# Performance work log

Measured on AMD Instinct MI355X. Metric: run time of the kernel, lower is better.

The kernel has to match this reference:

```python
import jax, jax.numpy as jnp
import numpy as np

N_HEADS = 32
N_KV_HEADS = 8
HEAD_DIM = 64  # dim // n_heads = 2048 // 32

def setup_inputs() -> dict:
    key = jax.random.key(0)
    k1, k2, k3, k4, k5 = jax.random.split(key, 5)
    B, T, D = 2, 2048, 2048
    s = 0.02
    return {
        "x": jax.random.normal(k1, (B, T, D), dtype=jnp.float32),
        "wq": jax.random.normal(k2, (D, D), dtype=jnp.float32) * s,
        "wk": jax.random.normal(k3, (N_KV_HEADS * HEAD_DIM, D), dtype=jnp.float32) * s,
        "wv": jax.random.normal(k4, (N_KV_HEADS * HEAD_DIM, D), dtype=jnp.float32) * s,
        "wo": jax.random.normal(k5, (D, D), dtype=jnp.float32) * s,
    }

def reference(x, wq, wk, wv, wo):
    B, T, D = x.shape
    ratio = N_HEADS // N_KV_HEADS
    scale = HEAD_DIM ** -0.5
    # projections (nn.Linear: x @ W.T)
    q = (x @ wq.T).reshape(B, T, N_HEADS, HEAD_DIM)
    k = (x @ wk.T).reshape(B, T, N_KV_HEADS, HEAD_DIM)
    v = (x @ wv.T).reshape(B, T, N_KV_HEADS, HEAD_DIM)
    # GQA expand: [B,T,kvh,d] -> [B,T,kvh*ratio,d]
    k = jnp.broadcast_to(k[:, :, :, None, :], (B, T, N_KV_HEADS, ratio, HEAD_DIM)).reshape(B, T, N_HEADS, HEAD_DIM)
    v = jnp.broadcast_to(v[:, :, :, None, :], (B, T, N_KV_HEADS, ratio, HEAD_DIM)).reshape(B, T, N_HEADS, HEAD_DIM)
    # [B,H,T,d]
    q = q.transpose(0, 2, 1, 3)
    k = k.transpose(0, 2, 1, 3)
    v = v.transpose(0, 2, 1, 3)
    # naive full score matrix [B,H,T,T]
    score = jnp.einsum('bhqd,bhkd->bhqk', q, k) * scale
    causal = jnp.triu(jnp.full((T, T), -jnp.inf, dtype=score.dtype), k=1)
    score = score + causal
    # upcast to fp32 for softmax (matches score.float())
    attn = jax.nn.softmax(score.astype(jnp.float32), axis=-1)
    out = jnp.einsum('bhqk,bhkd->bhqd', attn, v.astype(jnp.float32)).astype(x.dtype)
    out = out.transpose(0, 2, 1, 3).reshape(B, T, N_HEADS * HEAD_DIM)
    return out @ wo.T
```

## Files before the change

### kernel.cpp

```cpp
#include <hip/hip_runtime.h>
#include <hip/hip_bf16.h>

typedef unsigned short u16;
typedef unsigned int   u32;
typedef __attribute__((ext_vector_type(8))) short s16x8;
typedef __attribute__((ext_vector_type(4))) float f32x4;

__device__ __forceinline__ u16 f2bf(float f) {
    u32 u = __float_as_uint(f);
    u += 0x7fff + ((u >> 16) & 1);
    return (u16)(u >> 16);
}

__device__ __forceinline__ f32x4 mfma16(s16x8 a, s16x8 b, f32x4 c) {
    return __builtin_amdgcn_mfma_f32_16x16x32_bf16(a, b, c, 0, 0, 0);
}

#define GLL16(g, l)                                                            \
    __builtin_amdgcn_global_load_lds(                                          \
        (const __attribute__((address_space(1))) void*)(g),                    \
        (__attribute__((address_space(3))) void*)(l), 16, 0, 0)

__global__ void cvt_f32_bf16(const float* __restrict__ src, u16* __restrict__ dst, int n8) {
    int i = blockIdx.x * blockDim.x + threadIdx.x;
    if (i >= n8) return;
    const float4* s4 = reinterpret_cast<const float4*>(src);
    float4 a = s4[2 * i], b = s4[2 * i + 1];
    s16x8 o;
    o[0] = (short)f2bf(a.x); o[1] = (short)f2bf(a.y);
    o[2] = (short)f2bf(a.z); o[3] = (short)f2bf(a.w);
    o[4] = (short)f2bf(b.x); o[5] = (short)f2bf(b.y);
    o[6] = (short)f2bf(b.z); o[7] = (short)f2bf(b.w);
    reinterpret_cast<s16x8*>(dst)[i] = o;
}

template <int BF16_OUT>
__global__ __launch_bounds__(256, 2)
void gemm_bt(const u16* __restrict__ A, const u16* __restrict__ B,
             void* __restrict__ Cout, int M, int N, int K) {
    __shared__ __align__(16) u16 As[128 * 32];
    __shared__ __align__(16) u16 Bs[128 * 32];
    const int tid = threadIdx.x;
    const int w = tid >> 6, ln = tid & 63;
    const int m0 = blockIdx.y * 128, n0 = blockIdx.x * 128;
    const int wr = w >> 1, wc = w & 1;
    const int g = ln >> 4, c15 = ln & 15;
    f32x4 acc[4][4] = {};
    const int srow0 = w * 32 + (ln >> 2);
    const int spos = ln & 3;
    for (int k0 = 0; k0 < K; k0 += 32) {
        __syncthreads();
#pragma unroll
        for (int j = 0; j < 2; ++j) {
            int row = srow0 + j * 16;
            int ch = spos ^ ((row >> 1) & 3);
            const u16* ga = A + (size_t)(m0 + row) * K + k0 + ch * 8;
            GLL16(ga, (char*)As + (w * 32 + j * 16) * 64);
            const u16* gb = B + (size_t)(n0 + row) * K + k0 + ch * 8;
            GLL16(gb, (char*)Bs + (w * 32 + j * 16) * 64);
        }
        __syncthreads();
        s16x8 af[4], bfr[4];
#pragma unroll
        for (int ms = 0; ms < 4; ++ms) {
            int row = wr * 64 + ms * 16 + c15;
            int cp = g ^ ((row >> 1) & 3);
            af[ms] = *reinterpret_cast<const s16x8*>((const char*)As + row * 64 + cp * 16);
        }
#pragma unroll
        for (int ns = 0; ns < 4; ++ns) {
            int row = wc * 64 + ns * 16 + c15;
            int cp = g ^ ((row >> 1) & 3);
            bfr[ns] = *reinterpret_cast<const s16x8*>((const char*)Bs + row * 64 + cp * 16);
        }
        __builtin_amdgcn_s_setprio(1);
#pragma unroll
        for (int ms = 0; ms < 4; ++ms)
#pragma unroll
            for (int ns = 0; ns < 4; ++ns)
                acc[ms][ns] = mfma16(af[ms], bfr[ns], acc[ms][ns]);
        __builtin_amdgcn_s_setprio(0);
    }
#pragma unroll
    for (int ms = 0; ms < 4; ++ms)
#pragma unroll
        for (int ns = 0; ns < 4; ++ns)
#pragma unroll
            for (int r = 0; r < 4; ++r) {
                int row = m0 + wr * 64 + ms * 16 + g * 4 + r;
                int col = n0 + wc * 64 + ns * 16 + c15;
                float v = acc[ms][ns][r];
                if (BF16_OUT)
                    ((u16*)Cout)[(size_t)row * N + col] = f2bf(v);
                else
                    ((float*)Cout)[(size_t)row * N + col] = v;
            }
}

__global__ __launch_bounds__(512, 2)
void attn_fwd(const u16* __restrict__ qkv, u16* __restrict__ outp) {
    const int T = 2048, RS = 3072;
    const int pair = blockIdx.x, kvh = blockIdx.y, b = blockIdx.z;
    const int tid = threadIdx.x, w = tid >> 6, ln = tid & 63;
    const int g = ln >> 4, c15 = ln & 15;
    const int h = kvh * 4 + (w >> 1);
    const int qs = w & 1;
    __shared__ __align__(16) u16 Ks[64 * 64];
    __shared__ __align__(16) u16 Vt[64 * 72];
    __shared__ __align__(16) u16 Ps[8][32 * 72];
    const size_t base = (size_t)b * T * RS;
    const float SCALE2 = 0.125f * 1.44269504088896f;

    for (int ph = 0; ph < 2; ++ph) {
        const int qb = ph ? (31 - pair) : pair;
        const int qg0 = qb * 64 + qs * 32;

        s16x8 qf[2][2];
#pragma unroll
        for (int ms = 0; ms < 2; ++ms)
#pragma unroll
            for (int ks = 0; ks < 2; ++ks)
                qf[ms][ks] = *reinterpret_cast<const s16x8*>(
                    qkv + base + (size_t)(qg0 + ms * 16 + c15) * RS + h * 64 + ks * 32 + g * 8);

        f32x4 o[2][4] = {};
        float mrow[2][4], lrow[2][4];
#pragma unroll
        for (int ms = 0; ms < 2; ++ms)
#pragma unroll
            for (int r = 0; r < 4; ++r) { mrow[ms][r] = -INFINITY; lrow[ms][r] = 0.f; }

        const int nt = qb + 1;
        for (int t = 0; t < nt; ++t) {
            __syncthreads();
            {
                int row = w * 8 + (ln >> 3);
                int ch = (ln & 7) ^ (row & 7);
                const u16* gk = qkv + base + (size_t)(t * 64 + row) * RS + 2048 + kvh * 64 + ch * 8;
                GLL16(gk, (char*)Ks + w * 1024);
            }
            {
                s16x8 vv = *reinterpret_cast<const s16x8*>(
                    qkv + base + (size_t)(t * 64 + ln) * RS + 2560 + kvh * 64 + w * 8);
#pragma unroll
                for (int i = 0; i < 8; ++i)
                    Vt[(w * 8 + i) * 72 + ln] = (u16)vv[i];
            }
            __syncthreads();

            f32x4 s[2][4] = {};
#pragma unroll
            for (int ks = 0; ks < 2; ++ks) {
                s16x8 kf[4];
#pragma unroll
                for (int ns = 0; ns < 4; ++ns) {
                    int row = ns * 16 + c15;
                    int ch = (ks * 4 + g) ^ (row & 7);
                    kf[ns] = *reinterpret_cast<const s16x8*>((const char*)Ks + row * 128 + ch * 16);
                }
                __builtin_amdgcn_s_setprio(1);
#pragma unroll
                for (int ms = 0; ms < 2; ++ms)
#pragma unroll
                    for (int ns = 0; ns < 4; ++ns)
                        s[ms][ns] = mfma16(qf[ms][ks], kf[ns], s[ms][ns]);
                __builtin_amdgcn_s_setprio(0);
            }

#pragma unroll
            for (int ms = 0; ms < 2; ++ms) {
#pragma unroll
                for (int r = 0; r < 4; ++r) {
                    int qrow = qg0 + ms * 16 + g * 4 + r;
                    float mx = -INFINITY;
#pragma unroll
                    for (int ns = 0; ns < 4; ++ns) {
                        int col = t * 64 + ns * 16 + c15;
                        float v = s[ms][ns][r] * SCALE2;
                        v = (col <= qrow) ? v : -INFINITY;
                        s[ms][ns][r] = v;
                        mx = fmaxf(mx, v);
                    }
                    mx = fmaxf(mx, __shfl_xor(mx, 1));
                    mx = fmaxf(mx, __shfl_xor(mx, 2));
                    mx = fmaxf(mx, __shfl_xor(mx, 4));
                    mx = fmaxf(mx, __shfl_xor(mx, 8));
                    float mold = mrow[ms][r];
                    float mnew = fmaxf(mold, mx);
                    float fac = exp2f(mold - mnew);
                    float rsum = 0.f;
#pragma unroll
                    for (int ns = 0; ns < 4; ++ns) {
                        float p = exp2f(s[ms][ns][r] - mnew);
                        s[ms][ns][r] = p;
                        rsum += p;
                    }
                    rsum += __shfl_xor(rsum, 1);
                    rsum += __shfl_xor(rsum, 2);
                    rsum += __shfl_xor(rsum, 4);
                    rsum += __shfl_xor(rsum, 8);
                    mrow[ms][r] = mnew;
                    lrow[ms][r] = lrow[ms][r] * fac + rsum;
#pragma unroll
                    for (int ds = 0; ds < 4; ++ds) o[ms][ds][r] *= fac;
#pragma unroll
                    for (int ns = 0; ns < 4; ++ns)
                        Ps[w][(ms * 16 + g * 4 + r) * 72 + ns * 16 + c15] = f2bf(s[ms][ns][r]);
                }
            }
            __syncthreads();

#pragma unroll
            for (int ks = 0; ks < 2; ++ks) {
                s16x8 pf[2], vf[4];
#pragma unroll
                for (int ms = 0; ms < 2; ++ms)
                    pf[ms] = *reinterpret_cast<const s16x8*>(&Ps[w][(ms * 16 + c15) * 72 + ks * 32 + g * 8]);
#pragma unroll
                for (int ds = 0; ds < 4; ++ds)
                    vf[ds] = *reinterpret_cast<const s16x8*>(&Vt[(ds * 16 + c15) * 72 + ks * 32 + g * 8]);
                __builtin_amdgcn_s_setprio(1);
#pragma unroll
                for (int ms = 0; ms < 2; ++ms)
#pragma unroll
                    for (int ds = 0; ds < 4; ++ds)
                        o[ms][ds] = mfma16(pf[ms], vf[ds], o[ms][ds]);
                __builtin_amdgcn_s_setprio(0);
            }
        }

#pragma unroll
        for (int ms = 0; ms < 2; ++ms)
#pragma unroll
            for (int r = 0; r < 4; ++r) {
                float inv = 1.0f / lrow[ms][r];
                int qrow = qg0 + ms * 16 + g * 4 + r;
#pragma unroll
                for (int ds = 0; ds < 4; ++ds)
                    outp[(size_t)(b * T + qrow) * 2048 + h * 64 + ds * 16 + c15] =
                        f2bf(o[ms][ds][r] * inv);
            }
    }
}

extern "C" void kernel_launch(void* const* d_in, const int* in_sizes, int n_in,
                              void* d_out, int out_size, void* d_ws, size_t ws_size,
                              hipStream_t stream) {
    const float* x  = (const float*)d_in[0];
    const float* wq = (const float*)d_in[1];
    const float* wk = (const float*)d_in[2];
    const float* wv = (const float*)d_in[3];
    const float* wo = (const float*)d_in[4];

    u16* xb   = (u16*)d_ws;
    u16* wqkv = xb + 8388608;
    u16* wob  = wqkv + 6291456;
    u16* qkvb = wob + 4194304;
    u16* attb = qkvb + 12582912;

    cvt_f32_bf16<<<4096, 256, 0, stream>>>(x, xb, 1048576);
    cvt_f32_bf16<<<2048, 256, 0, stream>>>(wq, wqkv, 524288);
    cvt_f32_bf16<<<512, 256, 0, stream>>>(wk, wqkv + 2048 * 2048, 131072);
    cvt_f32_bf16<<<512, 256, 0, stream>>>(wv, wqkv + 2560 * 2048, 131072);
    cvt_f32_bf16<<<2048, 256, 0, stream>>>(wo, wob, 524288);

    gemm_bt<1><<<dim3(24, 32), 256, 0, stream>>>(xb, wqkv, qkvb, 4096, 3072, 2048);
    attn_fwd<<<dim3(16, 8, 2), 512, 0, stream>>>(qkvb, attb);
    gemm_bt<0><<<dim3(16, 32), 256, 0, stream>>>(attb, wob, d_out, 4096, 2048, 2048);
}
```

Before: 376.8 us.

## Restructure attention to 128-key tiles with lazy rescale and fused weight conversion

The attention kernel now uses 4 waves per block, with each wave owning one head over a 32-query tile. It processes 128-key tiles per iteration, which doubles the grid to 32 pair blocks. Causal masking runs only on the last tile, the online-softmax rescale is skipped unless the max grows past a threshold, and the row-sum shuffle reduction moves to the end. One block-wide barrier per tile is removed. The four weight conversion launches are merged into one kernel, and some bf16 conversions switch to the library intrinsic. The lazy rescale risks fp32 overflow only for large score growth, and larger tiles add wasted masked work on the diagonal.

```diff
diff --git a/kernel.cpp b/kernel.cpp
--- a/kernel.cpp
+++ b/kernel.cpp
@@ -10,6 +10,11 @@
     u32 u = __float_as_uint(f);
     u += 0x7fff + ((u >> 16) & 1);
     return (u16)(u >> 16);
+}
+
+__device__ __forceinline__ u16 f2bf_fast(float f) {
+    __hip_bfloat16 h = __float2bfloat16(f);
+    return *reinterpret_cast<u16*>(&h);
 }
 
 __device__ __forceinline__ f32x4 mfma16(s16x8 a, s16x8 b, f32x4 c) {
@@ -32,6 +37,25 @@
     o[4] = (short)f2bf(b.x); o[5] = (short)f2bf(b.y);
     o[6] = (short)f2bf(b.z); o[7] = (short)f2bf(b.w);
     reinterpret_cast<s16x8*>(dst)[i] = o;
+}
+
+__global__ void cvt_weights(const float* __restrict__ wq, const float* __restrict__ wk,
+                            const float* __restrict__ wv, const float* __restrict__ wo,
+                            u16* __restrict__ wqkv, u16* __restrict__ wob) {
+    int i = blockIdx.x * blockDim.x + threadIdx.x;
+    const float* src; u16* dst;
+    if (i < 524288)       { src = wq + (size_t)i * 8;            dst = wqkv + (size_t)i * 8; }
+    else if (i < 655360)  { int j = i - 524288; src = wk + (size_t)j * 8; dst = wqkv + 4194304 + (size_t)j * 8; }
+    else if (i < 786432)  { int j = i - 655360; src = wv + (size_t)j * 8; dst = wqkv + 5242880 + (size_t)j * 8; }
+    else                  { int j = i - 786432; src = wo + (size_t)j * 8; dst = wob + (size_t)j * 8; }
+    const float4* s4 = reinterpret_cast<const float4*>(src);
+    float4 a = s4[0], b = s4[1];
+    s16x8 o;
+    o[0] = (short)f2bf(a.x); o[1] = (short)f2bf(a.y);
+    o[2] = (short)f2bf(a.z); o[3] = (short)f2bf(a.w);
+    o[4] = (short)f2bf(b.x); o[5] = (short)f2bf(b.y);
+    o[6] = (short)f2bf(b.z); o[7] = (short)f2bf(b.w);
+    *reinterpret_cast<s16x8*>(dst) = o;
 }
 
 template <int BF16_OUT>
@@ -97,23 +121,23 @@
             }
 }
 
-__global__ __launch_bounds__(512, 2)
+__global__ __launch_bounds__(256, 2)
 void attn_fwd(const u16* __restrict__ qkv, u16* __restrict__ outp) {
     const int T = 2048, RS = 3072;
-    const int pair = blockIdx.x, kvh = blockIdx.y, b = blockIdx.z;
+    const int pr = blockIdx.x, kvh = blockIdx.y, b = blockIdx.z;
     const int tid = threadIdx.x, w = tid >> 6, ln = tid & 63;
     const int g = ln >> 4, c15 = ln & 15;
-    const int h = kvh * 4 + (w >> 1);
-    const int qs = w & 1;
-    __shared__ __align__(16) u16 Ks[64 * 64];
-    __shared__ __align__(16) u16 Vt[64 * 72];
-    __shared__ __align__(16) u16 Ps[8][32 * 72];
+    const int h = kvh * 4 + w;
+    __shared__ __align__(16) u16 Ks[128 * 64];
+    __shared__ __align__(16) u16 Vt[64 * 136];
+    __shared__ __align__(16) u16 Ps[4][32 * 72];
     const size_t base = (size_t)b * T * RS;
     const float SCALE2 = 0.125f * 1.44269504088896f;
+    const float THR = 8.0f;
 
     for (int ph = 0; ph < 2; ++ph) {
-        const int qb = ph ? (31 - pair) : pair;
-        const int qg0 = qb * 64 + qs * 32;
+        const int qt = ph ? (63 - pr) : pr;
+        const int qg0 = qt * 32;
 
         s16x8 qf[2][2];
 #pragma unroll
@@ -130,86 +154,119 @@
 #pragma unroll
             for (int r = 0; r < 4; ++r) { mrow[ms][r] = -INFINITY; lrow[ms][r] = 0.f; }
 
-        const int nt = qb + 1;
+        const int nt = (qt >> 2) + 1;
         for (int t = 0; t < nt; ++t) {
             __syncthreads();
-            {
-                int row = w * 8 + (ln >> 3);
+#pragma unroll
+            for (int j = 0; j < 4; ++j) {
+                int row = w * 32 + j * 8 + (ln >> 3);
                 int ch = (ln & 7) ^ (row & 7);
-                const u16* gk = qkv + base + (size_t)(t * 64 + row) * RS + 2048 + kvh * 64 + ch * 8;
-                GLL16(gk, (char*)Ks + w * 1024);
-            }
-            {
+                const u16* gk = qkv + base + (size_t)(t * 128 + row) * RS + 2048 + kvh * 64 + ch * 8;
+                GLL16(gk, (char*)Ks + (w * 32 + j * 8) * 128);
+            }
+#pragma unroll
+            for (int j = 0; j < 4; ++j) {
+                int cid = tid + j * 256;
+                int kv = cid & 127, dch = cid >> 7;
                 s16x8 vv = *reinterpret_cast<const s16x8*>(
-                    qkv + base + (size_t)(t * 64 + ln) * RS + 2560 + kvh * 64 + w * 8);
+                    qkv + base + (size_t)(t * 128 + kv) * RS + 2560 + kvh * 64 + dch * 8);
 #pragma unroll
                 for (int i = 0; i < 8; ++i)
-                    Vt[(w * 8 + i) * 72 + ln] = (u16)vv[i];
+                    Vt[(dch * 8 + i) * 136 + kv] = (u16)vv[i];
             }
             __syncthreads();
 
-            f32x4 s[2][4] = {};
-#pragma unroll
-            for (int ks = 0; ks < 2; ++ks) {
-                s16x8 kf[4];
-#pragma unroll
-                for (int ns = 0; ns < 4; ++ns) {
-                    int row = ns * 16 + c15;
-                    int ch = (ks * 4 + g) ^ (row & 7);
-                    kf[ns] = *reinterpret_cast<const s16x8*>((const char*)Ks + row * 128 + ch * 16);
+            f32x4 s[2][8] = {};
+#pragma unroll
+            for (int ks = 0; ks < 2; ++ks)
+#pragma unroll
+                for (int nh = 0; nh < 2; ++nh) {
+                    s16x8 kf[4];
+#pragma unroll
+                    for (int n4 = 0; n4 < 4; ++n4) {
+                        int row = (nh * 4 + n4) * 16 + c15;
+                        int ch = (ks * 4 + g) ^ (row & 7);
+                        kf[n4] = *reinterpret_cast<const s16x8*>((const char*)Ks + row * 128 + ch * 16);
+                    }
+                    __builtin_amdgcn_s_setprio(1);
+#pragma unroll
+                    for (int ms = 0; ms < 2; ++ms)
+#pragma unroll
+                        for (int n4 = 0; n4 < 4; ++n4)
+                            s[ms][nh * 4 + n4] = mfma16(qf[ms][ks], kf[n4], s[ms][nh * 4 + n4]);
+                    __builtin_amdgcn_s_setprio(0);
                 }
-                __builtin_amdgcn_s_setprio(1);
-#pragma unroll
-                for (int ms = 0; ms < 2; ++ms)
-#pragma unroll
-                    for (int ns = 0; ns < 4; ++ns)
-                        s[ms][ns] = mfma16(qf[ms][ks], kf[ns], s[ms][ns]);
-                __builtin_amdgcn_s_setprio(0);
-            }
-
-#pragma unroll
-            for (int ms = 0; ms < 2; ++ms) {
+
+            const bool lastT = (t == nt - 1);
+            float mx2[2][4];
+#pragma unroll
+            for (int ms = 0; ms < 2; ++ms)
 #pragma unroll
                 for (int r = 0; r < 4; ++r) {
-                    int qrow = qg0 + ms * 16 + g * 4 + r;
                     float mx = -INFINITY;
-#pragma unroll
-                    for (int ns = 0; ns < 4; ++ns) {
-                        int col = t * 64 + ns * 16 + c15;
-                        float v = s[ms][ns][r] * SCALE2;
-                        v = (col <= qrow) ? v : -INFINITY;
-                        s[ms][ns][r] = v;
-                        mx = fmaxf(mx, v);
+                    if (lastT) {
+                        int qrow = qg0 + ms * 16 + g * 4 + r;
+#pragma unroll
+                        for (int ns = 0; ns < 8; ++ns) {
+                            int col = t * 128 + ns * 16 + c15;
+                            float v = s[ms][ns][r] * SCALE2;
+                            v = (col <= qrow) ? v : -INFINITY;
+                            s[ms][ns][r] = v;
+                            mx = fmaxf(mx, v);
+                        }
+                    } else {
+#pragma unroll
+                        for (int ns = 0; ns < 8; ++ns) {
+                            float v = s[ms][ns][r] * SCALE2;
+                            s[ms][ns][r] = v;
+                            mx = fmaxf(mx, v);
+                        }
                     }
                     mx = fmaxf(mx, __shfl_xor(mx, 1));
                     mx = fmaxf(mx, __shfl_xor(mx, 2));
                     mx = fmaxf(mx, __shfl_xor(mx, 4));
                     mx = fmaxf(mx, __shfl_xor(mx, 8));
-                    float mold = mrow[ms][r];
-                    float mnew = fmaxf(mold, mx);
-                    float fac = exp2f(mold - mnew);
-                    float rsum = 0.f;
-#pragma unroll
-                    for (int ns = 0; ns < 4; ++ns) {
-                        float p = exp2f(s[ms][ns][r] - mnew);
+                    mx2[ms][r] = mx;
+                }
+
+            float growth = -INFINITY;
+#pragma unroll
+            for (int ms = 0; ms < 2; ++ms)
+#pragma unroll
+                for (int r = 0; r < 4; ++r)
+                    growth = fmaxf(growth, mx2[ms][r] - mrow[ms][r]);
+            if (__any(growth > THR)) {
+#pragma unroll
+                for (int ms = 0; ms < 2; ++ms)
+#pragma unroll
+                    for (int r = 0; r < 4; ++r) {
+                        float mnew = fmaxf(mrow[ms][r], mx2[ms][r]);
+                        float fac = exp2f(mrow[ms][r] - mnew);
+                        mrow[ms][r] = mnew;
+                        lrow[ms][r] *= fac;
+#pragma unroll
+                        for (int ds = 0; ds < 4; ++ds) o[ms][ds][r] *= fac;
+                    }
+            }
+
+#pragma unroll
+            for (int ms = 0; ms < 2; ++ms)
+#pragma unroll
+                for (int r = 0; r < 4; ++r) {
+                    float m = mrow[ms][r];
+                    float rs = 0.f;
+#pragma unroll
+                    for (int ns = 0; ns < 8; ++ns) {
+                        float p = exp2f(s[ms][ns][r] - m);
                         s[ms][ns][r] = p;
-                        rsum += p;
+                        rs += p;
                     }
-                    rsum += __shfl_xor(rsum, 1);
-                    rsum += __shfl_xor(rsum, 2);
-                    rsum += __shfl_xor(rsum, 4);
-                    rsum += __shfl_xor(rsum, 8);
-                    mrow[ms][r] = mnew;
-                    lrow[ms][r] = lrow[ms][r] * fac + rsum;
-#pragma unroll
-                    for (int ds = 0; ds < 4; ++ds) o[ms][ds][r] *= fac;
+                    lrow[ms][r] += rs;
+                    int prow = ms * 16 + g * 4 + r;
 #pragma unroll
                     for (int ns = 0; ns < 4; ++ns)
-                        Ps[w][(ms * 16 + g * 4 + r) * 72 + ns * 16 + c15] = f2bf(s[ms][ns][r]);
+                        Ps[w][prow * 72 + ns * 16 + c15] = f2bf_fast(s[ms][ns][r]);
                 }
-            }
-            __syncthreads();
-
 #pragma unroll
             for (int ks = 0; ks < 2; ++ks) {
                 s16x8 pf[2], vf[4];
@@ -218,7 +275,7 @@
                     pf[ms] = *reinterpret_cast<const s16x8*>(&Ps[w][(ms * 16 + c15) * 72 + ks * 32 + g * 8]);
 #pragma unroll
                 for (int ds = 0; ds < 4; ++ds)
-                    vf[ds] = *reinterpret_cast<const s16x8*>(&Vt[(ds * 16 + c15) * 72 + ks * 32 + g * 8]);
+                    vf[ds] = *reinterpret_cast<const s16x8*>(&Vt[(ds * 16 + c15) * 136 + ks * 32 + g * 8]);
                 __builtin_amdgcn_s_setprio(1);
 #pragma unroll
                 for (int ms = 0; ms < 2; ++ms)
@@ -227,18 +284,49 @@
                         o[ms][ds] = mfma16(pf[ms], vf[ds], o[ms][ds]);
                 __builtin_amdgcn_s_setprio(0);
             }
+#pragma unroll
+            for (int ms = 0; ms < 2; ++ms)
+#pragma unroll
+                for (int r = 0; r < 4; ++r) {
+                    int prow = ms * 16 + g * 4 + r;
+#pragma unroll
+                    for (int ns = 0; ns < 4; ++ns)
+                        Ps[w][prow * 72 + ns * 16 + c15] = f2bf_fast(s[ms][ns + 4][r]);
+                }
+#pragma unroll
+            for (int ks = 2; ks < 4; ++ks) {
+                s16x8 pf[2], vf[4];
+#pragma unroll
+                for (int ms = 0; ms < 2; ++ms)
+                    pf[ms] = *reinterpret_cast<const s16x8*>(&Ps[w][(ms * 16 + c15) * 72 + (ks - 2) * 32 + g * 8]);
+#pragma unroll
+                for (int ds = 0; ds < 4; ++ds)
+                    vf[ds] = *reinterpret_cast<const s16x8*>(&Vt[(ds * 16 + c15) * 136 + ks * 32 + g * 8]);
+                __builtin_amdgcn_s_setprio(1);
+#pragma unroll
+                for (int ms = 0; ms < 2; ++ms)
+#pragma unroll
+                    for (int ds = 0; ds < 4; ++ds)
+                        o[ms][ds] = mfma16(pf[ms], vf[ds], o[ms][ds]);
+                __builtin_amdgcn_s_setprio(0);
+            }
         }
 
 #pragma unroll
         for (int ms = 0; ms < 2; ++ms)
 #pragma unroll
             for (int r = 0; r < 4; ++r) {
-                float inv = 1.0f / lrow[ms][r];
+                float l = lrow[ms][r];
+                l += __shfl_xor(l, 1);
+                l += __shfl_xor(l, 2);
+                l += __shfl_xor(l, 4);
+                l += __shfl_xor(l, 8);
+                float inv = 1.0f / l;
                 int qrow = qg0 + ms * 16 + g * 4 + r;
 #pragma unroll
                 for (int ds = 0; ds < 4; ++ds)
                     outp[(size_t)(b * T + qrow) * 2048 + h * 64 + ds * 16 + c15] =
-                        f2bf(o[ms][ds][r] * inv);
+                        f2bf_fast(o[ms][ds][r] * inv);
             }
     }
 }
@@ -259,12 +347,9 @@
     u16* attb = qkvb + 12582912;
 
     cvt_f32_bf16<<<4096, 256, 0, stream>>>(x, xb, 1048576);
-    cvt_f32_bf16<<<2048, 256, 0, stream>>>(wq, wqkv, 524288);
-    cvt_f32_bf16<<<512, 256, 0, stream>>>(wk, wqkv + 2048 * 2048, 131072);
-    cvt_f32_bf16<<<512, 256, 0, stream>>>(wv, wqkv + 2560 * 2048, 131072);
-    cvt_f32_bf16<<<2048, 256, 0, stream>>>(wo, wob, 524288);
+    cvt_weights<<<5120, 256, 0, stream>>>(wq, wk, wv, wo, wqkv, wob);
 
     gemm_bt<1><<<dim3(24, 32), 256, 0, stream>>>(xb, wqkv, qkvb, 4096, 3072, 2048);
-    attn_fwd<<<dim3(16, 8, 2), 512, 0, stream>>>(qkvb, attb);
+    attn_fwd<<<dim3(32, 8, 2), 256, 0, stream>>>(qkvb, attb);
     gemm_bt<0><<<dim3(16, 32), 256, 0, stream>>>(attb, wob, d_out, 4096, 2048, 2048);
 }
```

Result: faster. 331.1 us (-12.1%).
